# Optimization experiments

Measured on AMD Instinct MI355X. Metric: run time of the kernel, lower is better.

Reference implementation:

```python
import jax, jax.numpy as jnp
import numpy as np
import math

S, B, H, NH = 2048, 2, 2048, 16
HN = H // NH  # head dim = 128

def setup_inputs() -> dict:
    key = jax.random.key(0)
    ks = jax.random.split(key, 5)
    hidden_states = jax.random.normal(ks[0], (S, B, H), dtype=jnp.float32)
    # causal mask: True means masked (filled with -10000), broadcast over heads
    attention_mask = jnp.triu(jnp.ones((S, S), dtype=bool), k=1)[None, None].repeat(B, axis=0)
    w_qkv = jax.random.normal(ks[1], (3 * H, H), dtype=jnp.float32) * (1.0 / math.sqrt(H))
    b_qkv = jax.random.normal(ks[2], (3 * H,), dtype=jnp.float32) * 0.02
    w_dense = jax.random.normal(ks[3], (H, H), dtype=jnp.float32) * (1.0 / math.sqrt(H))
    b_dense = jax.random.normal(ks[4], (H,), dtype=jnp.float32) * 0.02
    return {"hidden_states": hidden_states, "attention_mask": attention_mask,
            "w_qkv": w_qkv, "b_qkv": b_qkv, "w_dense": w_dense, "b_dense": b_dense}

def reference(hidden_states, attention_mask, w_qkv, b_qkv, w_dense, b_dense):
    s, b, h = hidden_states.shape
    nh, hn = NH, h // NH
    # QKV projection (ColumnParallelLinear, world_size=1)
    qkv = hidden_states @ w_qkv.T + b_qkv                # [s, b, 3h]
    qkv = qkv.reshape(s, b, nh, 3 * hn)
    q, k, v = jnp.split(qkv, 3, axis=-1)                 # each [s, b, nh, hn]
    q = q.transpose(1, 2, 0, 3)                          # [b, nh, s, hn]
    k = k.transpose(1, 2, 0, 3)
    v = v.transpose(1, 2, 0, 3)
    # norm_factor = sqrt(hn)*coeff, softmax rescales by coeff -> net 1/sqrt(hn)
    scores = jnp.einsum('bnqh,bnkh->bnqk', q, k) / jnp.float32(math.sqrt(hn))
    scores = jnp.where(attention_mask, jnp.float32(-10000.0), scores)
    probs = jax.nn.softmax(scores, axis=-1)              # [b, nh, s, s]
    ctx = jnp.einsum('bnqk,bnkh->bnqh', probs, v)        # [b, nh, s, hn]
    ctx = ctx.transpose(2, 0, 1, 3).reshape(s, b, h)     # [s, b, h]
    # RowParallelLinear with skip_bias_add=True: bias returned separately
    output = ctx @ w_dense.T
    return output, b_dense
```

## Files before the change

### kernel.cpp

```cpp
#include <hip/hip_runtime.h>

typedef unsigned short u16;
typedef unsigned int   u32;
typedef __attribute__((ext_vector_type(8))) short bf16x8;
typedef __attribute__((ext_vector_type(4))) float f32x4;

#define S_LEN 2048
#define B_SZ  2
#define H_DIM 2048
#define NH_   16
#define HN_   128
#define M_TOK 4096
#define NQKV  6144
#define NT_   (S_LEN / 64)

#define BAR      asm volatile("s_barrier" ::: "memory")
#define WAITV(n) asm volatile("s_waitcnt vmcnt(" #n ")" ::: "memory")

__device__ __forceinline__ u16 f2bf(float f) {
    u32 x = __float_as_uint(f);
    return (u16)((x + 0x7fffu + ((x >> 16) & 1u)) >> 16);
}

__device__ __forceinline__ void async16(const void* g, void* l) {
    __builtin_amdgcn_global_load_lds((const __attribute__((address_space(1))) void*)g,
                                     (__attribute__((address_space(3))) void*)l,
                                     16, 0, 0);
}

__global__ __launch_bounds__(256) void cvt3(
    const float* __restrict__ a, u16* __restrict__ oa, int na,
    const float* __restrict__ b, u16* __restrict__ ob, int nb,
    const float* __restrict__ c, u16* __restrict__ oc, int nc)
{
    int g = blockIdx.x * 256 + threadIdx.x;
    const float* in; u16* out; int idx;
    if (g < na)           { in = a; out = oa; idx = g; }
    else if (g < na + nb) { in = b; out = ob; idx = g - na; }
    else if (g < na + nb + nc) { in = c; out = oc; idx = g - na - nb; }
    else return;
    int i = idx * 4;
    float4 v = *(const float4*)&in[i];
    ushort4 o;
    o.x = f2bf(v.x); o.y = f2bf(v.y); o.z = f2bf(v.z); o.w = f2bf(v.w);
    *(ushort4*)&out[i] = o;
}

template<int EPI, int MM, int NN>
__global__ __launch_bounds__(512, 2) void gemm8(
    const u16* __restrict__ A, const u16* __restrict__ W,
    const float* __restrict__ bias, float* __restrict__ Cout,
    u16* __restrict__ Qb, u16* __restrict__ Kb, u16* __restrict__ Vt)
{
    constexpr int K   = 2048;
    constexpr int NKT = K / 64;
    constexpr int NBN = NN / 256;
    constexpr int NWG = (MM / 256) * NBN;

    __shared__ __align__(16) u16 sA[2][256 * 64];
    __shared__ __align__(16) u16 sB[2][256 * 64];

    const int t = threadIdx.x, l = t & 63, w = t >> 6;
    const int quad = l >> 4, ln = l & 15;
    const int qw_r = w >> 2, qw_c = w & 3;

    int wg = blockIdx.x;
    wg = (wg & 7) * (NWG / 8) + (wg >> 3);
    const int m0 = (wg / NBN) * 256, n0 = (wg % NBN) * 256;

    const int srow = t >> 3;
    const int skc  = (t & 7) ^ (srow & 7);
    const u16* pA = A + (size_t)(m0 + srow) * K + skc * 8;
    const u16* pB = W + (size_t)(n0 + srow) * K + skc * 8;

#define STAGE_A(db, h, kt)                                                        \
    do {                                                                          \
        async16(pA + (size_t)(h) * 128 * K + (size_t)(kt) * 64,                   \
                &sA[db][(h) * 8192 + t * 8]);                                     \
        async16(pA + (size_t)(h) * 128 * K + (size_t)64 * K + (size_t)(kt) * 64,  \
                &sA[db][(h) * 8192 + t * 8 + 4096]);                              \
    } while (0)
#define STAGE_B(db, h, kt)                                                        \
    do {                                                                          \
        async16(pB + (size_t)(h) * 128 * K + (size_t)(kt) * 64,                   \
                &sB[db][(h) * 8192 + t * 8]);                                     \
        async16(pB + (size_t)(h) * 128 * K + (size_t)64 * K + (size_t)(kt) * 64,  \
                &sB[db][(h) * 8192 + t * 8 + 4096]);                              \
    } while (0)

    const int aBase = (qw_r * 64 + ln) * 64;
    const int bBase = (qw_c * 32 + ln) * 64;
    int swz[2];
#pragma unroll
    for (int ks = 0; ks < 2; ++ks)
        swz[ks] = ((ks * 4 + quad) ^ (ln & 7)) << 3;

    bf16x8 af[4][2];
    bf16x8 bf[2][2];

#define RD_A(db, mq)                                                              \
    do {                                                                          \
        _Pragma("unroll") for (int mf = 0; mf < 4; ++mf)                          \
        _Pragma("unroll") for (int ks = 0; ks < 2; ++ks)                          \
            af[mf][ks] = *(const bf16x8*)&sA[db][aBase + (mq) * 8192 + mf * 1024  \
                                                + swz[ks]];                       \
    } while (0)
#define RD_B(db, nq)                                                              \
    do {                                                                          \
        _Pragma("unroll") for (int nf = 0; nf < 2; ++nf)                          \
        _Pragma("unroll") for (int ks = 0; ks < 2; ++ks)                          \
            bf[nf][ks] = *(const bf16x8*)&sB[db][bBase + (nq) * 8192 + nf * 1024  \
                                                + swz[ks]];                       \
    } while (0)

    f32x4 acc[4][4][2];
#pragma unroll
    for (int q = 0; q < 4; ++q)
#pragma unroll
        for (int mf = 0; mf < 4; ++mf)
#pragma unroll
            for (int nf = 0; nf < 2; ++nf)
#pragma unroll
                for (int r = 0; r < 4; ++r) acc[q][mf][nf][r] = 0.f;

#define MM16(q)                                                                   \
    do {                                                                          \
        __builtin_amdgcn_s_setprio(1);                                            \
        _Pragma("unroll") for (int mf = 0; mf < 4; ++mf)                          \
        _Pragma("unroll") for (int nf = 0; nf < 2; ++nf)                          \
        _Pragma("unroll") for (int ks = 0; ks < 2; ++ks)                          \
            acc[q][mf][nf] = __builtin_amdgcn_mfma_f32_16x16x32_bf16(             \
                af[mf][ks], bf[nf][ks], acc[q][mf][nf], 0, 0, 0);                 \
        __builtin_amdgcn_s_setprio(0);                                            \
    } while (0)

    STAGE_A(0, 0, 0); STAGE_B(0, 0, 0); STAGE_A(0, 1, 0); STAGE_B(0, 1, 0);
    STAGE_A(1, 0, 1); STAGE_B(1, 0, 1);
    WAITV(4);
    BAR;

#pragma unroll 1
    for (int i = 0; i < NKT / 2; ++i) {
        const int tt  = 2 * i;
        const int tp1 = tt + 1;
        const int tp2 = (tt + 2) & (NKT - 1);
        const int tp3 = (tt + 3) & (NKT - 1);

        RD_A(0, 0); RD_B(0, 0);
        STAGE_A(1, 1, tp1);
        BAR; MM16(0); BAR;
        RD_B(0, 1);
        STAGE_B(1, 1, tp1);
        BAR; MM16(1); BAR;
        RD_A(0, 1); RD_B(0, 0);
        STAGE_A(0, 0, tp2);
        BAR; MM16(2); BAR;
        RD_B(0, 1);
        STAGE_B(0, 0, tp2);
        BAR; MM16(3);
        WAITV(4);
        BAR;
        RD_A(1, 0); RD_B(1, 0);
        STAGE_A(0, 1, tp2);
        BAR; MM16(0); BAR;
        RD_B(1, 1);
        STAGE_B(0, 1, tp2);
        BAR; MM16(1); BAR;
        RD_A(1, 1); RD_B(1, 0);
        STAGE_A(1, 0, tp3);
        BAR; MM16(2); BAR;
        RD_B(1, 1);
        STAGE_B(1, 0, tp3);
        BAR; MM16(3);
        WAITV(4);
        BAR;
    }
#undef STAGE_A
#undef STAGE_B
#undef RD_A
#undef RD_B
#undef MM16

    if constexpr (EPI == 0) {
#pragma unroll
        for (int q = 0; q < 4; ++q) {
            const int mq = q >> 1, nq = q & 1;
#pragma unroll
            for (int mf = 0; mf < 4; ++mf)
#pragma unroll
                for (int nf = 0; nf < 2; ++nf) {
                    int col = n0 + nq * 128 + qw_c * 32 + nf * 16 + ln;
#pragma unroll
                    for (int r = 0; r < 4; ++r) {
                        int row = m0 + mq * 128 + qw_r * 64 + mf * 16 + quad * 4 + r;
                        Cout[(size_t)row * NN + col] = acc[q][mf][nf][r];
                    }
                }
        }
    } else {
        const float kQS = 0.08838834764831845f * 1.44269504088896340f;
#pragma unroll
        for (int q = 0; q < 4; ++q) {
            const int mq = q >> 1, nq = q & 1;
#pragma unroll
            for (int nf = 0; nf < 2; ++nf) {
                int col  = n0 + nq * 128 + qw_c * 32 + nf * 16 + ln;
                int head = col / 384;
                int g    = col - head * 384;
                int sec  = g >> 7;
                int d    = g & 127;
                float bv = bias[col];
#pragma unroll
                for (int mf = 0; mf < 4; ++mf)
#pragma unroll
                    for (int r = 0; r < 4; ++r) {
                        int tok = m0 + mq * 128 + qw_r * 64 + mf * 16 + quad * 4 + r;
                        int s = tok >> 1, bb = tok & 1;
                        float v = acc[q][mf][nf][r] + bv;
                        if (sec == 0)
                            Qb[((size_t)(bb * NH_ + head) * S_LEN + s) * HN_ + d] = f2bf(v * kQS);
                        else if (sec == 1)
                            Kb[((size_t)(bb * NH_ + head) * S_LEN + s) * HN_ + d] = f2bf(v);
                        else
                            Vt[((size_t)(bb * NH_ + head) * HN_ + d) * S_LEN + s] = f2bf(v);
                    }
            }
        }
    }
}

__global__ __launch_bounds__(256) void attn_mfma(
    const u16* __restrict__ Qb, const u16* __restrict__ Kb,
    const u16* __restrict__ Vt, u16* __restrict__ Ctx)
{
    __shared__ __align__(16) u16 Ks[2][16 * 64 * 8];
    __shared__ __align__(16) u16 Vs[2][16 * 64 * 8];
    __shared__ __align__(16) u16 Psm[4][16][72];

    const int t = threadIdx.x, l = t & 63, w = t >> 6;
    const int quad = l >> 4, ln = l & 15;
    const int j = blockIdx.x;
    const int n = blockIdx.y, b = blockIdx.z;
    const u16* Qh = Qb + (size_t)(b * NH_ + n) * S_LEN * HN_;
    const u16* Kh = Kb + (size_t)(b * NH_ + n) * S_LEN * HN_;
    const u16* Vh = Vt + (size_t)(b * NH_ + n) * HN_ * S_LEN;

#pragma unroll 1
    for (int phase = 0; phase < 2; ++phase) {
        const int qt = phase ? j : (NT_ - 1 - j);
        const int q0 = qt * 64;

#pragma unroll
        for (int i = 0; i < 4; ++i)
            async16(&Qh[(size_t)(q0 + i * 16 + ln) * HN_ + w * 32 + quad * 8],
                    &Ks[1][((i * 4 + w) * 64 + l) * 8]);
#pragma unroll
        for (int i = 0; i < 4; ++i) {
            async16(&Kh[(size_t)(i * 16 + ln) * HN_ + w * 32 + quad * 8],
                    &Ks[0][((i * 4 + w) * 64 + l) * 8]);
            int dv = i * 4 + w, dt = dv >> 1, ks = dv & 1;
            async16(&Vh[(size_t)(dt * 16 + ln) * S_LEN + ks * 32 + quad * 8],
                    &Vs[0][(dv * 64 + l) * 8]);
        }
        __syncthreads();

        bf16x8 qf[4];
#pragma unroll
        for (int ks = 0; ks < 4; ++ks)
            qf[ks] = *(const bf16x8*)&Ks[1][((w * 4 + ks) * 64 + l) * 8];
        __syncthreads();

        float m_i[4], l_i[4];
        f32x4 acco[8];
#pragma unroll
        for (int r = 0; r < 4; ++r) { m_i[r] = -1e30f; l_i[r] = 0.f; }
#pragma unroll
        for (int dt = 0; dt < 8; ++dt)
#pragma unroll
            for (int r = 0; r < 4; ++r) acco[dt][r] = 0.f;

#pragma unroll 1
        for (int kt = 0; kt <= qt; ++kt) {
            const int cur = kt & 1;

            if (kt < qt) {
                const int nxt = cur ^ 1;
#pragma unroll
                for (int i = 0; i < 4; ++i) {
                    async16(&Kh[(size_t)((kt + 1) * 64 + i * 16 + ln) * HN_ + w * 32 + quad * 8],
                            &Ks[nxt][((i * 4 + w) * 64 + l) * 8]);
                    int dv = i * 4 + w, dt = dv >> 1, ks = dv & 1;
                    async16(&Vh[(size_t)(dt * 16 + ln) * S_LEN + (kt + 1) * 64 + ks * 32 + quad * 8],
                            &Vs[nxt][(dv * 64 + l) * 8]);
                }
            }

            f32x4 sc[4];
#pragma unroll
            for (int nt = 0; nt < 4; ++nt)
#pragma unroll
                for (int r = 0; r < 4; ++r) sc[nt][r] = 0.f;
#pragma unroll
            for (int nt = 0; nt < 4; ++nt)
#pragma unroll
                for (int ks = 0; ks < 4; ++ks) {
                    bf16x8 kf = *(const bf16x8*)&Ks[cur][((nt * 4 + ks) * 64 + l) * 8];
                    sc[nt] = __builtin_amdgcn_mfma_f32_16x16x32_bf16(qf[ks], kf, sc[nt], 0, 0, 0);
                }

            if (kt == qt) {
#pragma unroll
                for (int nt = 0; nt < 4; ++nt)
#pragma unroll
                    for (int r = 0; r < 4; ++r)
                        if (nt * 16 + ln > w * 16 + quad * 4 + r) sc[nt][r] = -1e30f;
            }

            float corr[4];
#pragma unroll
            for (int r = 0; r < 4; ++r) {
                float mx = fmaxf(fmaxf(sc[0][r], sc[1][r]), fmaxf(sc[2][r], sc[3][r]));
                mx = fmaxf(mx, __shfl_xor(mx, 1));
                mx = fmaxf(mx, __shfl_xor(mx, 2));
                mx = fmaxf(mx, __shfl_xor(mx, 4));
                mx = fmaxf(mx, __shfl_xor(mx, 8));
                float mnew = fmaxf(m_i[r], mx);
                corr[r] = exp2f(m_i[r] - mnew);
                m_i[r] = mnew;
            }
#pragma unroll
            for (int r = 0; r < 4; ++r) {
                float ps = 0.f;
#pragma unroll
                for (int nt = 0; nt < 4; ++nt) {
                    float p = exp2f(sc[nt][r] - m_i[r]);
                    ps += p;
                    Psm[w][quad * 4 + r][nt * 16 + ln] = f2bf(p);
                }
                l_i[r] = l_i[r] * corr[r] + ps;
            }

#pragma unroll
            for (int dt = 0; dt < 8; ++dt)
#pragma unroll
                for (int r = 0; r < 4; ++r) acco[dt][r] *= corr[r];

            bf16x8 pf[2];
#pragma unroll
            for (int ks = 0; ks < 2; ++ks)
                pf[ks] = *(const bf16x8*)&Psm[w][ln][ks * 32 + quad * 8];
#pragma unroll
            for (int dt = 0; dt < 8; ++dt)
#pragma unroll
                for (int ks = 0; ks < 2; ++ks) {
                    bf16x8 vf = *(const bf16x8*)&Vs[cur][((dt * 2 + ks) * 64 + l) * 8];
                    acco[dt] = __builtin_amdgcn_mfma_f32_16x16x32_bf16(pf[ks], vf, acco[dt], 0, 0, 0);
                }
            __syncthreads();
        }

#pragma unroll
        for (int r = 0; r < 4; ++r) {
            float s = l_i[r];
            s += __shfl_xor(s, 1);
            s += __shfl_xor(s, 2);
            s += __shfl_xor(s, 4);
            s += __shfl_xor(s, 8);
            l_i[r] = 1.f / s;
        }
#pragma unroll
        for (int dt = 0; dt < 8; ++dt)
#pragma unroll
            for (int r = 0; r < 4; ++r) {
                int srow = q0 + w * 16 + quad * 4 + r;
                Ctx[((size_t)(srow * B_SZ + b)) * H_DIM + n * HN_ + dt * 16 + ln] =
                    f2bf(acco[dt][r] * l_i[r]);
            }
    }
}

__global__ void copy_bias(const float* __restrict__ b_dense, float* __restrict__ out)
{
    int t = blockIdx.x * 256 + threadIdx.x;
    if (t < H_DIM) out[(size_t)M_TOK * H_DIM + t] = b_dense[t];
}

extern "C" void kernel_launch(void* const* d_in, const int* in_sizes, int n_in,
                              void* d_out, int out_size, void* d_ws, size_t ws_size,
                              hipStream_t stream)
{
    const float* hs      = (const float*)d_in[0];
    const float* w_qkv   = (const float*)d_in[2];
    const float* b_qkv   = (const float*)d_in[3];
    const float* w_dense = (const float*)d_in[4];
    const float* b_dense = (const float*)d_in[5];
    float* out = (float*)d_out;

    u16* hs_bf = (u16*)d_ws;
    u16* wq_bf = hs_bf + (size_t)M_TOK * H_DIM;
    u16* wd_bf = wq_bf + (size_t)NQKV * H_DIM;
    u16* Qb    = wd_bf + (size_t)H_DIM * H_DIM;
    u16* Kb    = Qb    + (size_t)M_TOK * H_DIM;
    u16* Vt    = Kb    + (size_t)M_TOK * H_DIM;
    u16* Ctx   = Vt    + (size_t)M_TOK * H_DIM;

    const int g1 = (M_TOK * H_DIM) / 4;
    const int g2 = (NQKV * H_DIM) / 4;
    const int g3 = (H_DIM * H_DIM) / 4;
    cvt3<<<(g1 + g2 + g3 + 255) / 256, 256, 0, stream>>>(
        hs, hs_bf, g1, w_qkv, wq_bf, g2, w_dense, wd_bf, g3);

    gemm8<1, M_TOK, NQKV><<<(M_TOK / 256) * (NQKV / 256), 512, 0, stream>>>(
        hs_bf, wq_bf, b_qkv, nullptr, Qb, Kb, Vt);

    attn_mfma<<<dim3(NT_ / 2, NH_, B_SZ), 256, 0, stream>>>(Qb, Kb, Vt, Ctx);

    gemm8<0, M_TOK, H_DIM><<<(M_TOK / 256) * (H_DIM / 256), 512, 0, stream>>>(
        Ctx, wd_bf, nullptr, out, nullptr, nullptr, nullptr);

    copy_bias<<<(H_DIM + 255) / 256, 256, 0, stream>>>(b_dense, out);
}
```

Baseline: 450.4 us.

## Keep two B fragment sets in registers to cut redundant LDS reads in GEMM loop

The GEMM main loop now holds both B sub-tiles in separate register sets (bS0, bS1), so each B quarter is read from LDS once per k-tile instead of twice. The MFMA quadrant order becomes 0,1,3,2 and the global-to-LDS staging of B is rescheduled, with a deeper vmcnt wait. This cuts LDS traffic and removes one barrier pair per half-iteration, at the cost of extra VGPRs and a changed stage/wait ordering that must still be race-free.

```diff
diff --git a/kernel.cpp b/kernel.cpp
--- a/kernel.cpp
+++ b/kernel.cpp
@@ -96,7 +96,8 @@
         swz[ks] = ((ks * 4 + quad) ^ (ln & 7)) << 3;
 
     bf16x8 af[4][2];
-    bf16x8 bf[2][2];
+    bf16x8 bS0[2][2];
+    bf16x8 bS1[2][2];
 
 #define RD_A(db, mq)                                                              \
     do {                                                                          \
@@ -105,12 +106,12 @@
             af[mf][ks] = *(const bf16x8*)&sA[db][aBase + (mq) * 8192 + mf * 1024  \
                                                 + swz[ks]];                       \
     } while (0)
-#define RD_B(db, nq)                                                              \
+#define RD_B(db, nq, SET)                                                         \
     do {                                                                          \
         _Pragma("unroll") for (int nf = 0; nf < 2; ++nf)                          \
         _Pragma("unroll") for (int ks = 0; ks < 2; ++ks)                          \
-            bf[nf][ks] = *(const bf16x8*)&sB[db][bBase + (nq) * 8192 + nf * 1024  \
-                                                + swz[ks]];                       \
+            SET[nf][ks] = *(const bf16x8*)&sB[db][bBase + (nq) * 8192 + nf * 1024 \
+                                                 + swz[ks]];                      \
     } while (0)
 
     f32x4 acc[4][4][2];
@@ -123,20 +124,20 @@
 #pragma unroll
                 for (int r = 0; r < 4; ++r) acc[q][mf][nf][r] = 0.f;
 
-#define MM16(q)                                                                   \
+#define MM16(q, SET)                                                              \
     do {                                                                          \
         __builtin_amdgcn_s_setprio(1);                                            \
         _Pragma("unroll") for (int mf = 0; mf < 4; ++mf)                          \
         _Pragma("unroll") for (int nf = 0; nf < 2; ++nf)                          \
         _Pragma("unroll") for (int ks = 0; ks < 2; ++ks)                          \
             acc[q][mf][nf] = __builtin_amdgcn_mfma_f32_16x16x32_bf16(             \
-                af[mf][ks], bf[nf][ks], acc[q][mf][nf], 0, 0, 0);                 \
+                af[mf][ks], SET[nf][ks], acc[q][mf][nf], 0, 0, 0);                \
         __builtin_amdgcn_s_setprio(0);                                            \
     } while (0)
 
-    STAGE_A(0, 0, 0); STAGE_B(0, 0, 0); STAGE_A(0, 1, 0); STAGE_B(0, 1, 0);
-    STAGE_A(1, 0, 1); STAGE_B(1, 0, 1);
-    WAITV(4);
+    STAGE_A(0, 0, 0); STAGE_B(0, 0, 0); STAGE_B(0, 1, 0); STAGE_A(0, 1, 0);
+    STAGE_A(1, 0, 1); STAGE_B(1, 0, 1); STAGE_B(1, 1, 1);
+    WAITV(6);
     BAR;
 
 #pragma unroll 1
@@ -146,33 +147,31 @@
         const int tp2 = (tt + 2) & (NKT - 1);
         const int tp3 = (tt + 3) & (NKT - 1);
 
-        RD_A(0, 0); RD_B(0, 0);
+        RD_A(0, 0); RD_B(0, 0, bS0);
         STAGE_A(1, 1, tp1);
-        BAR; MM16(0); BAR;
-        RD_B(0, 1);
-        STAGE_B(1, 1, tp1);
-        BAR; MM16(1); BAR;
-        RD_A(0, 1); RD_B(0, 0);
+        BAR; MM16(0, bS0); BAR;
+        RD_B(0, 1, bS1);
         STAGE_A(0, 0, tp2);
-        BAR; MM16(2); BAR;
-        RD_B(0, 1);
+        BAR; MM16(1, bS1); BAR;
+        RD_A(0, 1);
         STAGE_B(0, 0, tp2);
-        BAR; MM16(3);
-        WAITV(4);
+        BAR; MM16(3, bS1); BAR;
+        STAGE_B(0, 1, tp2);
+        MM16(2, bS0);
+        WAITV(6);
         BAR;
-        RD_A(1, 0); RD_B(1, 0);
+        RD_A(1, 0); RD_B(1, 0, bS0);
         STAGE_A(0, 1, tp2);
-        BAR; MM16(0); BAR;
-        RD_B(1, 1);
-        STAGE_B(0, 1, tp2);
-        BAR; MM16(1); BAR;
-        RD_A(1, 1); RD_B(1, 0);
+        BAR; MM16(0, bS0); BAR;
+        RD_B(1, 1, bS1);
         STAGE_A(1, 0, tp3);
-        BAR; MM16(2); BAR;
-        RD_B(1, 1);
+        BAR; MM16(1, bS1); BAR;
+        RD_A(1, 1);
         STAGE_B(1, 0, tp3);
-        BAR; MM16(3);
-        WAITV(4);
+        BAR; MM16(3, bS1); BAR;
+        STAGE_B(1, 1, tp3);
+        MM16(2, bS0);
+        WAITV(6);
         BAR;
     }
 #undef STAGE_A
```

Result: faster. 429.0 us (-4.8%).
